# Optimization experiments

Hardware: AMD Instinct MI355X
Metric: run time of the kernel (lower is better)

## Reference

```python
import jax, jax.numpy as jnp
import numpy as np

B, IN_UNITS, IN_CH, NUM_UNITS, UNIT_SIZE = 32, 16, 2048, 16, 64
NUM_ITERS = 2


def setup_inputs() -> dict:
    key = jax.random.key(0)
    k1, k2 = jax.random.split(key)
    x = jax.random.normal(k1, (B, IN_UNITS, IN_CH), dtype=jnp.float32)
    W = jax.random.normal(k2, (1, IN_CH, NUM_UNITS, UNIT_SIZE, IN_UNITS), dtype=jnp.float32)
    return {"x": x, "W": W}


def squash(s):
    # torch code sums squared magnitude over dim=2 (the num_units axis) with keepdim
    mag_sq = jnp.sum(s * s, axis=2, keepdims=True)
    mag = jnp.sqrt(mag_sq)
    return mag_sq / (1.0 + mag_sq) * (s / mag)


def reference(x, W):
    # x: (B, in_units, in_channels) -> (B, in_channels, in_units)
    xt = jnp.swapaxes(x, 1, 2)
    # u_hat[b,i,j,k] = sum_u W[0,i,j,k,u] * xt[b,i,u]  -> (B, IC, NU, US)
    u_hat = jnp.einsum('ijku,biu->bijk', W[0], xt)
    b_ij = jnp.zeros((1, IN_CH, NUM_UNITS, 1), dtype=x.dtype)
    v_j = None
    for _ in range(NUM_ITERS):
        # softmax over a singleton trailing dim -> all ones (faithful to source)
        c_ij = jax.nn.softmax(b_ij, axis=-1)  # (1, IC, NU, 1), broadcasts over batch
        s_j = jnp.sum(c_ij[None, ..., 0][0][None].squeeze(0) * 0 + c_ij * u_hat, axis=1, keepdims=True) if False else jnp.sum(c_ij * u_hat, axis=1, keepdims=True)  # (B,1,NU,US)
        v_j = squash(s_j)  # (B,1,NU,US)
        # agreement: <u_hat, v_j> over unit_size, broadcast v_j over in_channels
        u_vj1 = jnp.einsum('bijk,bljk->bij', u_hat, v_j)  # (B, IC, NU)
        u_vj1 = jnp.mean(u_vj1, axis=0, keepdims=True)[..., None]  # (1, IC, NU, 1)
        b_ij = b_ij + u_vj1
    return v_j[:, 0, :, :]  # (B, num_units, unit_size)
```

## Files before the change

### kernel.cpp

```cpp
#include <hip/hip_runtime.h>
#include <hip/hip_bf16.h>


#define B_SZ   32
#define IC     2048
#define NJ     16
#define NK     64
#define SOUT   (B_SZ*NJ*NK)
#define KSTEPS 1024
#define KSPLIT 32
#define SPW    (KSTEPS/KSPLIT)

typedef float  v4f __attribute__((ext_vector_type(4)));
typedef short  v8s __attribute__((ext_vector_type(8)));
typedef uint   v4u __attribute__((ext_vector_type(4)));

static __device__ inline uint pk2(float a, float b) {
    __hip_bfloat162 h = __float22bfloat162_rn(make_float2(a, b));
    uint r;
    __builtin_memcpy(&r, &h, 4);
    return r;
}

__global__ __launch_bounds__(256)
void caps_xprep(const float* __restrict__ x, ushort* __restrict__ xb) {
    __shared__ ushort tile[256 * 18];
    const int t  = threadIdx.x;
    const int i0 = blockIdx.x * 16;
    const int mt = blockIdx.y;

    {
        const int r2 = t;
        const float* xp = x + (size_t)(mt * 256 + r2) * IC + i0;
        v4f f0 = *(const v4f*)(xp);
        v4f f1 = *(const v4f*)(xp + 4);
        v4f f2 = *(const v4f*)(xp + 8);
        v4f f3 = *(const v4f*)(xp + 12);
        uint d[8] = {pk2(f0.x, f0.y), pk2(f0.z, f0.w), pk2(f1.x, f1.y), pk2(f1.z, f1.w),
                     pk2(f2.x, f2.y), pk2(f2.z, f2.w), pk2(f3.x, f3.y), pk2(f3.z, f3.w)};
        const int swz = ((r2 >> 3) & 7) << 1;
        #pragma unroll
        for (int c = 0; c < 8; ++c)
            *(uint*)&tile[r2 * 18 + ((2 * c) ^ swz)] = d[c];
    }
    __syncthreads();

    #pragma unroll
    for (int rr = 0; rr < 2; ++rr) {
        const int idx   = rr * 256 + t;
        const int stepl = idx >> 6;
        const int lane  = idx & 63;
        const int q  = lane >> 4;
        const int bl = lane & 15;
        const int il = 2 * stepl + (q >> 1);
        const int rb = bl * 16 + (q & 1) * 8;
        const int swz = ((rb >> 3) & 7) << 1;
        ushort v[8];
        #pragma unroll
        for (int jj = 0; jj < 8; ++jj)
            v[jj] = tile[(rb + jj) * 18 + (il ^ swz)];
        const int stepg = blockIdx.x * 8 + stepl;
        *(v8s*)(xb + (size_t)stepg * 1024 + mt * 512 + lane * 8) = *(const v8s*)v;
    }
}

__global__ __launch_bounds__(256)
void caps_mfma(const ushort* __restrict__ xb, const float* __restrict__ W,
               float* __restrict__ part) {
    const int tid   = threadIdx.x;
    const int wv    = tid >> 6;
    const int lane  = tid & 63;
    const int j     = blockIdx.x;
    const int split = blockIdx.y;
    const int n     = lane & 15;
    const int q     = lane >> 4;
    const int step0 = split * SPW;

    v4f acc0 = {0.f, 0.f, 0.f, 0.f};
    v4f acc1 = {0.f, 0.f, 0.f, 0.f};

    const float*  wp = W + (size_t)(2 * step0 + (q >> 1)) * 16384
                         + (size_t)j * 1024 + (size_t)(wv * 16 + n) * 16 + (q & 1) * 8;
    const ushort* xp = xb + (size_t)step0 * 1024 + (size_t)lane * 8;

    #pragma unroll 4
    for (int s = 0; s < SPW; ++s) {
        v4f w0 = *(const v4f*)(wp);
        v4f w1 = *(const v4f*)(wp + 4);
        v8s a0 = *(const v8s*)(xp);
        v8s a1 = *(const v8s*)(xp + 512);
        v4u bu;
        bu[0] = pk2(w0.x, w0.y);
        bu[1] = pk2(w0.z, w0.w);
        bu[2] = pk2(w1.x, w1.y);
        bu[3] = pk2(w1.z, w1.w);
        v8s bb;
        __builtin_memcpy(&bb, &bu, 16);
        acc0 = __builtin_amdgcn_mfma_f32_16x16x32_bf16(a0, bb, acc0, 0, 0, 0);
        acc1 = __builtin_amdgcn_mfma_f32_16x16x32_bf16(a1, bb, acc1, 0, 0, 0);
        wp += 2 * 16384;
        xp += 1024;
    }

    float* pp = part + (size_t)split * SOUT + (size_t)j * NK + wv * 16 + n;
    #pragma unroll
    for (int r = 0; r < 4; ++r) {
        int m = q * 4 + r;
        pp[(size_t)m * 1024]        = acc0[r];
        pp[(size_t)(m + 16) * 1024] = acc1[r];
    }
}

__global__ __launch_bounds__(256)
void caps_finish(const float* __restrict__ part, float* __restrict__ out) {
    __shared__ float ls[256];
    __shared__ float l2[64];
    const int bid = blockIdx.x;
    const int b   = bid >> 4;
    const int k0  = (bid & 15) * 4;
    const int tid = threadIdx.x;
    const int jj  = tid >> 4;
    const int kc  = (tid >> 2) & 3;
    const int sg  = tid & 3;
    const size_t idx = (size_t)b * 1024 + (size_t)jj * NK + k0 + kc;

    float s = 0.0f;
    #pragma unroll
    for (int ss = 0; ss < KSPLIT / 4; ++ss)
        s += part[(size_t)(sg + 4 * ss) * SOUT + idx];
    ls[tid] = s;
    __syncthreads();

    if (sg == 0)
        l2[jj * 4 + kc] = ls[tid] + ls[tid + 1] + ls[tid + 2] + ls[tid + 3];
    __syncthreads();

    if (sg == 0) {
        float sa  = l2[jj * 4 + kc];
        float msq = 0.0f;
        #pragma unroll
        for (int j2 = 0; j2 < NJ; ++j2) {
            float v = l2[j2 * 4 + kc];
            msq += v * v;
        }
        float mag = sqrtf(msq);
        out[idx] = sa * (mag / (1.0f + msq));
    }
}

extern "C" void kernel_launch(void* const* d_in, const int* in_sizes, int n_in,
                              void* d_out, int out_size, void* d_ws, size_t ws_size,
                              hipStream_t stream) {
    const float* x = (const float*)d_in[0];
    const float* W = (const float*)d_in[1];
    float* out  = (float*)d_out;

    float*  part = (float*)d_ws;
    ushort* xb   = (ushort*)(part + (size_t)KSPLIT * SOUT);

    caps_xprep <<<dim3(128, 2),     256, 0, stream>>>(x, xb);
    caps_mfma  <<<dim3(NJ, KSPLIT), 256, 0, stream>>>(xb, W, part);
    caps_finish<<<512,              256, 0, stream>>>(part, out);
}
```

Measured before the change: 201.6 us.

## Double-buffer W and x tiles in LDS via async global_load_lds

```diff
diff --git a/kernel.cpp b/kernel.cpp
--- a/kernel.cpp
+++ b/kernel.cpp
@@ -67,6 +67,8 @@
 __global__ __launch_bounds__(256)
 void caps_mfma(const ushort* __restrict__ xb, const float* __restrict__ W,
                float* __restrict__ part) {
+    __shared__ float  ldsW[2][2048];
+    __shared__ ushort ldsX[2][1024];
     const int tid   = threadIdx.x;
     const int wv    = tid >> 6;
     const int lane  = tid & 63;
@@ -76,19 +78,47 @@
     const int q     = lane >> 4;
     const int step0 = split * SPW;
 
+    #define STAGE(s, b) do {                                                      \
+        const int m0 = wv * 2;                                                    \
+        const float* s0 = W + (size_t)(2 * (step0 + (s)) + (m0 >> 2)) * 16384     \
+                            + (size_t)j * 1024 + (m0 & 3) * 256 + lane * 4;       \
+        __builtin_amdgcn_global_load_lds((const void*)s0, (void*)&ldsW[b][m0*256],\
+                                         16, 0, 0);                               \
+        const int m1 = m0 + 1;                                                    \
+        const float* s1 = W + (size_t)(2 * (step0 + (s)) + (m1 >> 2)) * 16384     \
+                            + (size_t)j * 1024 + (m1 & 3) * 256 + lane * 4;       \
+        __builtin_amdgcn_global_load_lds((const void*)s1, (void*)&ldsW[b][m1*256],\
+                                         16, 0, 0);                               \
+        if (wv < 2) {                                                             \
+            const ushort* sx = xb + (size_t)(step0 + (s)) * 1024 + wv * 512       \
+                                  + lane * 8;                                     \
+            __builtin_amdgcn_global_load_lds((const void*)sx,                     \
+                                             (void*)&ldsX[b][wv*512], 16, 0, 0);  \
+        }                                                                         \
+    } while (0)
+
     v4f acc0 = {0.f, 0.f, 0.f, 0.f};
     v4f acc1 = {0.f, 0.f, 0.f, 0.f};
+    const int f0 = (q >> 1) * 1024 + (wv * 16 + n) * 16 + (q & 1) * 8;
 
-    const float*  wp = W + (size_t)(2 * step0 + (q >> 1)) * 16384
-                         + (size_t)j * 1024 + (size_t)(wv * 16 + n) * 16 + (q & 1) * 8;
-    const ushort* xp = xb + (size_t)step0 * 1024 + (size_t)lane * 8;
+    STAGE(0, 0);
+    #pragma unroll 1
+    for (int s = 0; s < SPW; ++s) {
+        const int cur = s & 1;
+        if (s + 1 < SPW) {
+            STAGE(s + 1, cur ^ 1);
+            if (wv < 2) asm volatile("s_waitcnt vmcnt(3)" ::: "memory");
+            else        asm volatile("s_waitcnt vmcnt(2)" ::: "memory");
+        } else {
+            asm volatile("s_waitcnt vmcnt(0)" ::: "memory");
+        }
+        __builtin_amdgcn_s_barrier();
+        __builtin_amdgcn_sched_barrier(0);
 
-    #pragma unroll 4
-    for (int s = 0; s < SPW; ++s) {
-        v4f w0 = *(const v4f*)(wp);
-        v4f w1 = *(const v4f*)(wp + 4);
-        v8s a0 = *(const v8s*)(xp);
-        v8s a1 = *(const v8s*)(xp + 512);
+        v4f w0 = *(const v4f*)&ldsW[cur][f0];
+        v4f w1 = *(const v4f*)&ldsW[cur][f0 + 4];
+        v8s a0 = *(const v8s*)&ldsX[cur][lane * 8];
+        v8s a1 = *(const v8s*)&ldsX[cur][512 + lane * 8];
         v4u bu;
         bu[0] = pk2(w0.x, w0.y);
         bu[1] = pk2(w0.z, w0.w);
@@ -98,9 +128,11 @@
         __builtin_memcpy(&bb, &bu, 16);
         acc0 = __builtin_amdgcn_mfma_f32_16x16x32_bf16(a0, bb, acc0, 0, 0, 0);
         acc1 = __builtin_amdgcn_mfma_f32_16x16x32_bf16(a1, bb, acc1, 0, 0, 0);
-        wp += 2 * 16384;
-        xp += 1024;
+
+        __builtin_amdgcn_sched_barrier(0);
+        __builtin_amdgcn_s_barrier();
     }
+    #undef STAGE
 
     float* pp = part + (size_t)split * SOUT + (size_t)j * NK + wv * 16 + n;
     #pragma unroll
```

Result: no change. 203.4 us (+0.9%).
